# Optimization experiments

Hardware: AMD Instinct MI355X
Metric: run time of the kernel (lower is better)

## Reference

```python
import jax, jax.numpy as jnp
import numpy as np

BG_W = 1.0
DILATED_BG_W = 5.0
EDGE_W = 20.0
KSIZE = 3


def setup_inputs() -> dict:
    key = jax.random.key(0)
    k1, k2 = jax.random.split(key)
    B, C, H, W = 16, 1, 1024, 1024
    pred = jax.random.normal(k1, (B, C, H, W), dtype=jnp.float32)
    target = (jax.random.uniform(k2, (B, C, H, W)) < 0.05).astype(jnp.float32)
    return {"pred": pred, "target": target}


def _dilate(target):
    # cv2.dilate with KSIZExKSIZE rect kernel == max pool, stride 1, SAME padding
    return jax.lax.reduce_window(
        target, -jnp.inf, jax.lax.max,
        window_dimensions=(1, 1, KSIZE, KSIZE),
        window_strides=(1, 1, 1, 1),
        padding="SAME",
    )


def reference(pred, target):
    dilated = _dilate(target)
    # weight: edge pixels (target>0.5) -> EDGE_W, else dilated band -> DILATED_BG_W, else BG_W
    weight = jnp.where(target > 0.5, EDGE_W,
                       jnp.where(dilated > 0.5, DILATED_BG_W, BG_W))
    # binary_cross_entropy_with_logits, reduction='none', then mean
    x = pred
    losses = weight * (jnp.maximum(x, 0.0) - x * target + jnp.log1p(jnp.exp(-jnp.abs(x))))
    return jnp.mean(losses)
```

## Files before the change

kernel.cpp:

```cpp
#include <hip/hip_runtime.h>

#define HH 1024
#define WW 1024
#define W4 (WW / 4)
#define ROWS 8

__device__ __forceinline__ float4 fmax4(float4 a, float4 b) {
    return make_float4(fmaxf(a.x, b.x), fmaxf(a.y, b.y),
                       fmaxf(a.z, b.z), fmaxf(a.w, b.w));
}

__device__ __forceinline__ float loss_elem(float x, float t, float dil) {
    float w = (t > 0.5f) ? 20.0f : ((dil > 0.5f) ? 5.0f : 1.0f);
    float a  = fabsf(x);
    float sp = __logf(1.0f + __expf(-a));
    return w * (fmaxf(x, 0.0f) - x * t + sp);
}

__global__ __launch_bounds__(256) void dilatedweightBCE_main(
        const float* __restrict__ pred,
        const float* __restrict__ target,
        float* __restrict__ partial) {
    __shared__ float swave[4];

    const int tid  = threadIdx.x;
    const int lane = tid & 63;
    const int c    = tid * 4;
    const int b    = blockIdx.y;
    const int h0   = blockIdx.x * ROWS;

    const float* timg = target + (size_t)b * HH * WW;
    const float4* tg  = (const float4*)timg;
    const float4* pg  = (const float4*)(pred + (size_t)b * HH * WW);

    const float4 zero = make_float4(0.0f, 0.0f, 0.0f, 0.0f);
    float4 t_prev = (h0 > 0) ? tg[(size_t)(h0 - 1) * W4 + tid] : zero;
    float4 t_cur  = tg[(size_t)h0 * W4 + tid];

    float s = 0.0f;
    #pragma unroll
    for (int r = 0; r < ROWS; ++r) {
        const int h = h0 + r;
        const bool has_up = (h > 0);
        const bool has_dn = (h < HH - 1);
        const size_t rowoff = (size_t)h * WW;

        float4 t_next = has_dn ? tg[(size_t)(h + 1) * W4 + tid] : zero;
        float4 x      = pg[(size_t)h * W4 + tid];

        float4 vm = fmax4(fmax4(t_prev, t_cur), t_next);

        float l  = __shfl_up(vm.w, 1);
        float rr = __shfl_down(vm.x, 1);

        if (lane == 0) {
            l = 0.0f;
            if (c > 0) {
                float v = timg[rowoff + c - 1];
                if (has_up) v = fmaxf(v, timg[rowoff - WW + c - 1]);
                if (has_dn) v = fmaxf(v, timg[rowoff + WW + c - 1]);
                l = v;
            }
        }
        if (lane == 63) {
            rr = 0.0f;
            if (c + 4 < WW) {
                float v = timg[rowoff + c + 4];
                if (has_up) v = fmaxf(v, timg[rowoff - WW + c + 4]);
                if (has_dn) v = fmaxf(v, timg[rowoff + WW + c + 4]);
                rr = v;
            }
        }

        float d0 = fmaxf(l,    fmaxf(vm.x, vm.y));
        float d1 = fmaxf(vm.x, fmaxf(vm.y, vm.z));
        float d2 = fmaxf(vm.y, fmaxf(vm.z, vm.w));
        float d3 = fmaxf(vm.z, fmaxf(vm.w, rr));

        s += loss_elem(x.x, t_cur.x, d0);
        s += loss_elem(x.y, t_cur.y, d1);
        s += loss_elem(x.z, t_cur.z, d2);
        s += loss_elem(x.w, t_cur.w, d3);

        t_prev = t_cur;
        t_cur  = t_next;
    }

    #pragma unroll
    for (int off = 32; off > 0; off >>= 1)
        s += __shfl_down(s, off);

    const int wave = tid >> 6;
    if (lane == 0) swave[wave] = s;
    __syncthreads();
    if (tid == 0) {
        partial[blockIdx.y * gridDim.x + blockIdx.x] =
            swave[0] + swave[1] + swave[2] + swave[3];
    }
}

__global__ __launch_bounds__(256) void dilatedweightBCE_reduce(
        const float* __restrict__ partial,
        float* __restrict__ out,
        int npart4,
        float inv_n) {
    __shared__ float swave[4];
    const int tid = threadIdx.x;

    float s = 0.0f;
    const float4* p4 = (const float4*)partial;
    for (int i = tid; i < npart4; i += 256) {
        float4 v = p4[i];
        s += v.x + v.y + v.z + v.w;
    }

    #pragma unroll
    for (int off = 32; off > 0; off >>= 1)
        s += __shfl_down(s, off);

    const int wave = tid >> 6;
    const int lane = tid & 63;
    if (lane == 0) swave[wave] = s;
    __syncthreads();
    if (tid == 0)
        out[0] = (swave[0] + swave[1] + swave[2] + swave[3]) * inv_n;
}

extern "C" void kernel_launch(void* const* d_in, const int* in_sizes, int n_in,
                              void* d_out, int out_size, void* d_ws, size_t ws_size,
                              hipStream_t stream) {
    const float* pred   = (const float*)d_in[0];
    const float* target = (const float*)d_in[1];
    float* out     = (float*)d_out;
    float* partial = (float*)d_ws;

    const int n  = in_sizes[0];
    const int Bn = n / (HH * WW);
    const int nblocks = (HH / ROWS) * Bn;

    dim3 grid(HH / ROWS, Bn);
    dilatedweightBCE_main<<<grid, 256, 0, stream>>>(pred, target, partial);
    dilatedweightBCE_reduce<<<1, 256, 0, stream>>>(partial, out,
                                                   nblocks / 4, 1.0f / (float)n);
}
```

Before: 162.6 us.

## Hoist all row loads up front and precompute halo columns per block

Each block now loads all target and pred rows, plus the two boundary rows, into registers before computing, so many loads are in flight at once. The per-row lane-0/lane-63 scalar halo loads are gathered into one batch per edge lane before the loop. Rows per block drop from 8 to 4, which doubles the grid and the number of partials. The cost is more redundant reads of halo rows (6 target rows per 4 rows of output) and higher register use.

```diff
diff --git a/kernel.cpp b/kernel.cpp
--- a/kernel.cpp
+++ b/kernel.cpp
@@ -3,11 +3,10 @@
 #define HH 1024
 #define WW 1024
 #define W4 (WW / 4)
-#define ROWS 8
+#define ROWS 4
 
-__device__ __forceinline__ float4 fmax4(float4 a, float4 b) {
-    return make_float4(fmaxf(a.x, b.x), fmaxf(a.y, b.y),
-                       fmaxf(a.z, b.z), fmaxf(a.w, b.w));
+__device__ __forceinline__ float fmax3(float a, float b, float c) {
+    return fmaxf(a, fmaxf(b, c));
 }
 
 __device__ __forceinline__ float loss_elem(float x, float t, float dil) {
@@ -32,58 +31,61 @@
     const float* timg = target + (size_t)b * HH * WW;
     const float4* tg  = (const float4*)timg;
     const float4* pg  = (const float4*)(pred + (size_t)b * HH * WW);
+    const float4 zero = make_float4(0.0f, 0.0f, 0.0f, 0.0f);
 
-    const float4 zero = make_float4(0.0f, 0.0f, 0.0f, 0.0f);
-    float4 t_prev = (h0 > 0) ? tg[(size_t)(h0 - 1) * W4 + tid] : zero;
-    float4 t_cur  = tg[(size_t)h0 * W4 + tid];
+    float4 tr[ROWS + 2];
+    tr[0] = (h0 > 0) ? tg[(size_t)(h0 - 1) * W4 + tid] : zero;
+    #pragma unroll
+    for (int r = 0; r < ROWS; ++r)
+        tr[r + 1] = tg[(size_t)(h0 + r) * W4 + tid];
+    tr[ROWS + 1] = (h0 + ROWS < HH) ? tg[(size_t)(h0 + ROWS) * W4 + tid] : zero;
+
+    float4 xr[ROWS];
+    #pragma unroll
+    for (int r = 0; r < ROWS; ++r)
+        xr[r] = pg[(size_t)(h0 + r) * W4 + tid];
+
+    float halo[ROWS];
+    #pragma unroll
+    for (int r = 0; r < ROWS; ++r) halo[r] = 0.0f;
+    if (lane == 0 || lane == 63) {
+        const int pc = (lane == 0) ? c - 1 : c + 4;
+        if (pc >= 0 && pc < WW) {
+            float pv[ROWS + 2];
+            pv[0] = (h0 > 0) ? timg[(size_t)(h0 - 1) * WW + pc] : 0.0f;
+            #pragma unroll
+            for (int r = 0; r < ROWS; ++r)
+                pv[r + 1] = timg[(size_t)(h0 + r) * WW + pc];
+            pv[ROWS + 1] = (h0 + ROWS < HH)
+                         ? timg[(size_t)(h0 + ROWS) * WW + pc] : 0.0f;
+            #pragma unroll
+            for (int r = 0; r < ROWS; ++r)
+                halo[r] = fmax3(pv[r], pv[r + 1], pv[r + 2]);
+        }
+    }
 
     float s = 0.0f;
     #pragma unroll
     for (int r = 0; r < ROWS; ++r) {
-        const int h = h0 + r;
-        const bool has_up = (h > 0);
-        const bool has_dn = (h < HH - 1);
-        const size_t rowoff = (size_t)h * WW;
-
-        float4 t_next = has_dn ? tg[(size_t)(h + 1) * W4 + tid] : zero;
-        float4 x      = pg[(size_t)h * W4 + tid];
-
-        float4 vm = fmax4(fmax4(t_prev, t_cur), t_next);
+        float4 a = tr[r], m = tr[r + 1], d = tr[r + 2];
+        float4 vm = make_float4(fmax3(a.x, m.x, d.x), fmax3(a.y, m.y, d.y),
+                                fmax3(a.z, m.z, d.z), fmax3(a.w, m.w, d.w));
 
         float l  = __shfl_up(vm.w, 1);
         float rr = __shfl_down(vm.x, 1);
+        if (lane == 0)  l  = halo[r];
+        if (lane == 63) rr = halo[r];
 
-        if (lane == 0) {
-            l = 0.0f;
-            if (c > 0) {
-                float v = timg[rowoff + c - 1];
-                if (has_up) v = fmaxf(v, timg[rowoff - WW + c - 1]);
-                if (has_dn) v = fmaxf(v, timg[rowoff + WW + c - 1]);
-                l = v;
-            }
-        }
-        if (lane == 63) {
-            rr = 0.0f;
-            if (c + 4 < WW) {
-                float v = timg[rowoff + c + 4];
-                if (has_up) v = fmaxf(v, timg[rowoff - WW + c + 4]);
-                if (has_dn) v = fmaxf(v, timg[rowoff + WW + c + 4]);
-                rr = v;
-            }
-        }
+        float d0 = fmax3(l,    vm.x, vm.y);
+        float d1 = fmax3(vm.x, vm.y, vm.z);
+        float d2 = fmax3(vm.y, vm.z, vm.w);
+        float d3 = fmax3(vm.z, vm.w, rr);
 
-        float d0 = fmaxf(l,    fmaxf(vm.x, vm.y));
-        float d1 = fmaxf(vm.x, fmaxf(vm.y, vm.z));
-        float d2 = fmaxf(vm.y, fmaxf(vm.z, vm.w));
-        float d3 = fmaxf(vm.z, fmaxf(vm.w, rr));
-
-        s += loss_elem(x.x, t_cur.x, d0);
-        s += loss_elem(x.y, t_cur.y, d1);
-        s += loss_elem(x.z, t_cur.z, d2);
-        s += loss_elem(x.w, t_cur.w, d3);
-
-        t_prev = t_cur;
-        t_cur  = t_next;
+        float4 x = xr[r];
+        s += loss_elem(x.x, m.x, d0);
+        s += loss_elem(x.y, m.y, d1);
+        s += loss_elem(x.z, m.z, d2);
+        s += loss_elem(x.w, m.w, d3);
     }
 
     #pragma unroll
```

Result: faster. 142.1 us (-12.6%).
